# Kernel optimization log

Measured on AMD Instinct MI355X. Metric: run time of the kernel, lower is better.

Reference implementation:

```python
import jax, jax.numpy as jnp
import numpy as np

N_NODES = 100000
N_EDGES = 1600000
IN_F = 256
OUT_F = 128


def setup_inputs() -> dict:
    key = jax.random.key(0)
    k1, k2, k3, k4, k5, k6 = jax.random.split(key, 6)
    X_input = jax.random.normal(k1, (N_NODES, IN_F), dtype=jnp.float32)
    adj_row = jax.random.randint(k2, (N_EDGES,), 0, N_NODES, dtype=jnp.int32)
    adj_col = jax.random.randint(k3, (N_EDGES,), 0, N_NODES, dtype=jnp.int32)
    adj_val = jax.random.uniform(k4, (N_EDGES,), dtype=jnp.float32)
    W = jax.random.normal(k5, (IN_F, OUT_F), dtype=jnp.float32) / np.sqrt(IN_F)
    bias = jax.random.normal(k6, (OUT_F,), dtype=jnp.float32) * 0.01
    return {"X_input": X_input, "adj_row": adj_row, "adj_col": adj_col,
            "adj_val": adj_val, "W": W, "bias": bias}


def reference(X_input, adj_row, adj_col, adj_val, W, bias):
    # dense linear (no bias): support = X @ W   [N, out]
    support = X_input @ W
    # sparse adjacency matmul (COO spmm): out[r] += val * support[c]
    messages = adj_val[:, None] * support[adj_col]          # [E, out]
    output = jax.ops.segment_sum(messages, adj_row, num_segments=N_NODES)
    return output + bias
```

## Files before the change

kernel.cpp:

```cpp
#include <hip/hip_runtime.h>

#define N_NODES 100000
#define N_EDGES 1600000
#define IN_F    256
#define OUT_F   128

#define BROWS    128
#define NB       782
#define CAP      2560
#define PART_EPB 8192

typedef __attribute__((ext_vector_type(8))) short   s16x8;
typedef __attribute__((ext_vector_type(4))) float   f32x4;
typedef __attribute__((ext_vector_type(8))) unsigned short u16x8;

__device__ __forceinline__ unsigned short f2bf(float f) {
    unsigned u = __float_as_uint(f);
    u += 0x7FFFu + ((u >> 16) & 1u);
    return (unsigned short)(u >> 16);
}
__device__ __forceinline__ float bf2f(unsigned short h) {
    return __uint_as_float((unsigned)h << 16);
}

__global__ __launch_bounds__(256) void wt_build(const float* __restrict__ W,
                                                unsigned short* __restrict__ Wt) {
    const int n = blockIdx.x;
    const int k = threadIdx.x;
    Wt[n * IN_F + k] = f2bf(W[(size_t)k * OUT_F + n]);
}

__global__ __launch_bounds__(256) void gemm_mfma(const float* __restrict__ X,
                                                 const unsigned short* __restrict__ Wt,
                                                 unsigned short* __restrict__ support) {
    __shared__ unsigned short As[64][40];
    __shared__ unsigned short Bs[128][40];
    __shared__ unsigned short Ct[64][136];

    const int t    = threadIdx.x;
    const int wid  = t >> 6;
    const int lane = t & 63;
    const int tm   = lane & 15;
    const int quad = lane >> 4;
    const int row0 = blockIdx.x * 64;

    f32x4 acc[8];
#pragma unroll
    for (int c = 0; c < 8; ++c) acc[c] = (f32x4){0.f, 0.f, 0.f, 0.f};

    for (int kb = 0; kb < IN_F; kb += 32) {
        {
            const int m  = t >> 2;
            const int k0 = (t & 3) * 8;
            const int gr = row0 + m;
            float4 x0 = make_float4(0.f, 0.f, 0.f, 0.f), x1 = x0;
            if (gr < N_NODES) {
                const float* xp = &X[(size_t)gr * IN_F + kb + k0];
                x0 = *(const float4*)xp;
                x1 = *(const float4*)(xp + 4);
            }
            ushort4 a0, a1;
            a0.x = f2bf(x0.x); a0.y = f2bf(x0.y); a0.z = f2bf(x0.z); a0.w = f2bf(x0.w);
            a1.x = f2bf(x1.x); a1.y = f2bf(x1.y); a1.z = f2bf(x1.z); a1.w = f2bf(x1.w);
            *(ushort4*)&As[m][k0]     = a0;
            *(ushort4*)&As[m][k0 + 4] = a1;
        }
        {
            const int n  = t >> 1;
            const int k0 = (t & 1) * 16;
            const unsigned short* wp = &Wt[(size_t)n * IN_F + kb + k0];
            *(u16x8*)&Bs[n][k0]     = *(const u16x8*)wp;
            *(u16x8*)&Bs[n][k0 + 8] = *(const u16x8*)(wp + 8);
        }
        __syncthreads();

        const s16x8 a = *(const s16x8*)&As[wid * 16 + tm][quad * 8];
#pragma unroll
        for (int c = 0; c < 8; ++c) {
            const s16x8 b = *(const s16x8*)&Bs[c * 16 + tm][quad * 8];
            acc[c] = __builtin_amdgcn_mfma_f32_16x16x32_bf16(a, b, acc[c], 0, 0, 0);
        }
        __syncthreads();
    }

#pragma unroll
    for (int c = 0; c < 8; ++c) {
        const int col = c * 16 + tm;
#pragma unroll
        for (int reg = 0; reg < 4; ++reg) {
            const int m = wid * 16 + quad * 4 + reg;
            Ct[m][col] = f2bf(acc[c][reg]);
        }
    }
    __syncthreads();
    {
        const int m   = t >> 2;
        const int seg = (t & 3) * 32;
        const int gr  = row0 + m;
        if (gr < N_NODES) {
            unsigned short* op = &support[(size_t)gr * OUT_F + seg];
#pragma unroll
            for (int i = 0; i < 4; ++i)
                *(u16x8*)(op + i * 8) = *(const u16x8*)&Ct[m][seg + i * 8];
        }
    }
}

__global__ __launch_bounds__(256) void zero_cursor(int* __restrict__ cursor) {
    const int i = blockIdx.x * 256 + threadIdx.x;
    if (i < NB) cursor[i] = 0;
}

__global__ __launch_bounds__(256) void partition_edges(const int* __restrict__ arow,
                                                       const int* __restrict__ acol,
                                                       const float* __restrict__ aval,
                                                       int* __restrict__ cursor,
                                                       int2* __restrict__ epackA) {
    __shared__ int cnt[NB];
    __shared__ int basep[NB];
    const int t = threadIdx.x;
    for (int k = t; k < NB; k += 256) cnt[k] = 0;
    __syncthreads();
    const int base = blockIdx.x * PART_EPB;
    const int lim  = min(base + PART_EPB, N_EDGES);
    for (int i = base + t; i < lim; i += 256) atomicAdd(&cnt[arow[i] >> 7], 1);
    __syncthreads();
    for (int k = t; k < NB; k += 256) {
        const int c = cnt[k];
        if (c > 0) basep[k] = atomicAdd(&cursor[k], c);
        cnt[k] = 0;
    }
    __syncthreads();
    for (int i = base + t; i < lim; i += 256) {
        const int r    = arow[i];
        const int b    = r >> 7;
        const int rank = atomicAdd(&cnt[b], 1);
        const int pos  = basep[b] + rank;
        if (pos < CAP)
            epackA[(size_t)b * CAP + pos] =
                make_int2(((r & (BROWS - 1)) << 17) | acol[i], __float_as_int(aval[i]));
    }
}

__global__ __launch_bounds__(256) void bucket_csr(const int* __restrict__ cursor,
                                                  const int2* __restrict__ epackA,
                                                  int2* __restrict__ rowmeta,
                                                  int2* __restrict__ epackB) {
    __shared__ int rcnt[BROWS];
    __shared__ int incl[BROWS];
    __shared__ int rcur[BROWS];
    const int b = blockIdx.x;
    const int t = threadIdx.x;
    const int s = b * CAP;
    const int n = min(cursor[b], CAP);

    if (t < BROWS) rcnt[t] = 0;
    __syncthreads();
    for (int i = t; i < n; i += 256) atomicAdd(&rcnt[epackA[s + i].x >> 17], 1);
    __syncthreads();

    if (t < BROWS) {
        const int lane = t & 63;
        int x = rcnt[t];
#pragma unroll
        for (int off = 1; off < 64; off <<= 1) {
            const int y = __shfl_up(x, off, 64);
            if (lane >= off) x += y;
        }
        incl[t] = x;
    }
    __syncthreads();
    if (t < BROWS) {
        const int excl = incl[t] - rcnt[t] + (t >= 64 ? incl[63] : 0);
        rcur[t] = excl;
        const int r = (b << 7) + t;
        if (r < N_NODES) rowmeta[r] = make_int2(s + excl, rcnt[t]);
    }
    __syncthreads();

    for (int i = t; i < n; i += 256) {
        const int2 ep  = epackA[s + i];
        const int  rl  = ep.x >> 17;
        const int  pos = atomicAdd(&rcur[rl], 1);
        epackB[s + pos] = make_int2(ep.x & 0x1FFFF, ep.y);
    }
}

__global__ __launch_bounds__(256) void csr_gather(const int2* __restrict__ rowmeta,
                                                  const int2* __restrict__ epackB,
                                                  const unsigned short* __restrict__ support,
                                                  const float* __restrict__ bias,
                                                  float* __restrict__ out) {
    const int t = threadIdx.x;
    const int g = t >> 5;
    const int l = t & 31;
    const int r = blockIdx.x * 8 + g;
    if (r >= N_NODES) return;

    const int2 rm   = rowmeta[r];
    const int start = rm.x;
    const int deg   = rm.y;

    float4 acc = *(const float4*)&bias[l * 4];

    int i = 0;
    for (; i + 4 <= deg; i += 4) {
        const int2 e0 = epackB[start + i + 0];
        const int2 e1 = epackB[start + i + 1];
        const int2 e2 = epackB[start + i + 2];
        const int2 e3 = epackB[start + i + 3];
        const ushort4 u0 = *(const ushort4*)&support[(size_t)e0.x * OUT_F + l * 4];
        const ushort4 u1 = *(const ushort4*)&support[(size_t)e1.x * OUT_F + l * 4];
        const ushort4 u2 = *(const ushort4*)&support[(size_t)e2.x * OUT_F + l * 4];
        const ushort4 u3 = *(const ushort4*)&support[(size_t)e3.x * OUT_F + l * 4];
        const float v0 = __int_as_float(e0.y);
        const float v1 = __int_as_float(e1.y);
        const float v2 = __int_as_float(e2.y);
        const float v3 = __int_as_float(e3.y);
        acc.x = fmaf(v0, bf2f(u0.x), fmaf(v1, bf2f(u1.x), fmaf(v2, bf2f(u2.x), fmaf(v3, bf2f(u3.x), acc.x))));
        acc.y = fmaf(v0, bf2f(u0.y), fmaf(v1, bf2f(u1.y), fmaf(v2, bf2f(u2.y), fmaf(v3, bf2f(u3.y), acc.y))));
        acc.z = fmaf(v0, bf2f(u0.z), fmaf(v1, bf2f(u1.z), fmaf(v2, bf2f(u2.z), fmaf(v3, bf2f(u3.z), acc.z))));
        acc.w = fmaf(v0, bf2f(u0.w), fmaf(v1, bf2f(u1.w), fmaf(v2, bf2f(u2.w), fmaf(v3, bf2f(u3.w), acc.w))));
    }
    for (; i < deg; ++i) {
        const int2 e = epackB[start + i];
        const ushort4 u = *(const ushort4*)&support[(size_t)e.x * OUT_F + l * 4];
        const float v = __int_as_float(e.y);
        acc.x = fmaf(v, bf2f(u.x), acc.x);
        acc.y = fmaf(v, bf2f(u.y), acc.y);
        acc.z = fmaf(v, bf2f(u.z), acc.z);
        acc.w = fmaf(v, bf2f(u.w), acc.w);
    }

    *(float4*)&out[(size_t)r * OUT_F + l * 4] = acc;
}

extern "C" void kernel_launch(void* const* d_in, const int* in_sizes, int n_in,
                              void* d_out, int out_size, void* d_ws, size_t ws_size,
                              hipStream_t stream) {
    const float* X    = (const float*)d_in[0];
    const int*   arow = (const int*)d_in[1];
    const int*   acol = (const int*)d_in[2];
    const float* aval = (const float*)d_in[3];
    const float* W    = (const float*)d_in[4];
    const float* bias = (const float*)d_in[5];
    float*       out  = (float*)d_out;

    char* ws = (char*)d_ws;
    unsigned short* support = (unsigned short*)ws;  ws += (size_t)N_NODES * OUT_F * 2;
    int2*  rowmeta = (int2*)ws;                     ws += (size_t)N_NODES * 8;
    unsigned short* Wt = (unsigned short*)ws;       ws += (size_t)IN_F * OUT_F * 2;
    int*   cursor  = (int*)ws;                      ws += ((NB + 7) & ~7) * 4;
    int2*  epackB  = (int2*)ws;
    int2*  epackA  = (int2*)d_out;

    wt_build<<<OUT_F, 256, 0, stream>>>(W, Wt);
    zero_cursor<<<4, 256, 0, stream>>>(cursor);
    gemm_mfma<<<(N_NODES + 63) / 64, 256, 0, stream>>>(X, Wt, support);
    partition_edges<<<(N_EDGES + PART_EPB - 1) / PART_EPB, 256, 0, stream>>>(
        arow, acol, aval, cursor, epackA);
    bucket_csr<<<NB, 256, 0, stream>>>(cursor, epackA, rowmeta, epackB);
    csr_gather<<<(N_NODES + 7) / 8, 256, 0, stream>>>(
        rowmeta, epackB, support, bias, out);
}
```

Before: 320.8 us.

## Build CSR via global row histogram, three-pass scan, and atomic scatter

Replaces the two-level bucket partition (bucket buckets of 128 rows with fixed capacity, then per-bucket sort) with a direct COO-to-CSR conversion. A global per-row histogram is built with atomics, then a three-kernel prefix scan produces row offsets, and edges are scattered to their final positions with global atomic cursors. This removes the intermediate epackA pass and the capacity cap, and it fuses zeroing of the row counters into wt_build. In exchange it adds more kernel launches and more global atomic traffic spread over 100k counters.

```diff
diff --git a/kernel.cpp b/kernel.cpp
--- a/kernel.cpp
+++ b/kernel.cpp
@@ -5,10 +5,9 @@
 #define IN_F    256
 #define OUT_F   128
 
-#define BROWS    128
-#define NB       782
-#define CAP      2560
-#define PART_EPB 8192
+#define NPAD      100352
+#define SCAN_NBLK 98
+#define HIST_EPB  4096
 
 typedef __attribute__((ext_vector_type(8))) short   s16x8;
 typedef __attribute__((ext_vector_type(4))) float   f32x4;
@@ -24,10 +23,13 @@
 }
 
 __global__ __launch_bounds__(256) void wt_build(const float* __restrict__ W,
-                                                unsigned short* __restrict__ Wt) {
+                                                unsigned short* __restrict__ Wt,
+                                                int* __restrict__ rowcnt) {
     const int n = blockIdx.x;
     const int k = threadIdx.x;
     Wt[n * IN_F + k] = f2bf(W[(size_t)k * OUT_F + n]);
+    for (int i = blockIdx.x * 256 + threadIdx.x; i < NPAD; i += OUT_F * 256)
+        rowcnt[i] = 0;
 }
 
 __global__ __launch_bounds__(256) void gemm_mfma(const float* __restrict__ X,
@@ -106,83 +108,95 @@
     }
 }
 
-__global__ __launch_bounds__(256) void zero_cursor(int* __restrict__ cursor) {
-    const int i = blockIdx.x * 256 + threadIdx.x;
-    if (i < NB) cursor[i] = 0;
-}
-
-__global__ __launch_bounds__(256) void partition_edges(const int* __restrict__ arow,
-                                                       const int* __restrict__ acol,
-                                                       const float* __restrict__ aval,
-                                                       int* __restrict__ cursor,
-                                                       int2* __restrict__ epackA) {
-    __shared__ int cnt[NB];
-    __shared__ int basep[NB];
-    const int t = threadIdx.x;
-    for (int k = t; k < NB; k += 256) cnt[k] = 0;
+__global__ __launch_bounds__(256) void hist(const int* __restrict__ arow,
+                                            int* __restrict__ rowcnt) {
+    const int base = blockIdx.x * HIST_EPB;
+    const int lim  = min(base + HIST_EPB, N_EDGES);
+    for (int i = base + threadIdx.x; i < lim; i += 256)
+        atomicAdd(&rowcnt[arow[i]], 1);
+}
+
+__global__ __launch_bounds__(256) void scan1(const int* __restrict__ rowcnt,
+                                             int* __restrict__ tmp,
+                                             int* __restrict__ btot) {
+    __shared__ int wsum[4];
+    const int t  = threadIdx.x;
+    const int i0 = blockIdx.x * 1024 + t * 4;
+    const int4 v = *(const int4*)&rowcnt[i0];
+    const int tsum = v.x + v.y + v.z + v.w;
+    const int lane = t & 63;
+    int x = tsum;
+#pragma unroll
+    for (int off = 1; off < 64; off <<= 1) {
+        const int y = __shfl_up(x, off, 64);
+        if (lane >= off) x += y;
+    }
+    if (lane == 63) wsum[t >> 6] = x;
     __syncthreads();
-    const int base = blockIdx.x * PART_EPB;
-    const int lim  = min(base + PART_EPB, N_EDGES);
-    for (int i = base + t; i < lim; i += 256) atomicAdd(&cnt[arow[i] >> 7], 1);
+    int pre = x - tsum;
+    const int w = t >> 6;
+    for (int k = 0; k < w; ++k) pre += wsum[k];
+    int4 o;
+    o.x = pre;
+    o.y = pre + v.x;
+    o.z = o.y + v.y;
+    o.w = o.z + v.z;
+    *(int4*)&tmp[i0] = o;
+    if (t == 255) btot[blockIdx.x] = pre + tsum;
+}
+
+__global__ __launch_bounds__(128) void scan2(const int* __restrict__ btot,
+                                             int* __restrict__ boffs) {
+    __shared__ int s[128];
+    const int t  = threadIdx.x;
+    const int my = (t < SCAN_NBLK) ? btot[t] : 0;
+    s[t] = my;
     __syncthreads();
-    for (int k = t; k < NB; k += 256) {
-        const int c = cnt[k];
-        if (c > 0) basep[k] = atomicAdd(&cursor[k], c);
-        cnt[k] = 0;
-    }
-    __syncthreads();
-    for (int i = base + t; i < lim; i += 256) {
-        const int r    = arow[i];
-        const int b    = r >> 7;
-        const int rank = atomicAdd(&cnt[b], 1);
-        const int pos  = basep[b] + rank;
-        if (pos < CAP)
-            epackA[(size_t)b * CAP + pos] =
-                make_int2(((r & (BROWS - 1)) << 17) | acol[i], __float_as_int(aval[i]));
-    }
-}
-
-__global__ __launch_bounds__(256) void bucket_csr(const int* __restrict__ cursor,
-                                                  const int2* __restrict__ epackA,
-                                                  int2* __restrict__ rowmeta,
-                                                  int2* __restrict__ epackB) {
-    __shared__ int rcnt[BROWS];
-    __shared__ int incl[BROWS];
-    __shared__ int rcur[BROWS];
-    const int b = blockIdx.x;
-    const int t = threadIdx.x;
-    const int s = b * CAP;
-    const int n = min(cursor[b], CAP);
-
-    if (t < BROWS) rcnt[t] = 0;
-    __syncthreads();
-    for (int i = t; i < n; i += 256) atomicAdd(&rcnt[epackA[s + i].x >> 17], 1);
-    __syncthreads();
-
-    if (t < BROWS) {
-        const int lane = t & 63;
-        int x = rcnt[t];
-#pragma unroll
-        for (int off = 1; off < 64; off <<= 1) {
-            const int y = __shfl_up(x, off, 64);
-            if (lane >= off) x += y;
-        }
-        incl[t] = x;
-    }
-    __syncthreads();
-    if (t < BROWS) {
-        const int excl = incl[t] - rcnt[t] + (t >= 64 ? incl[63] : 0);
-        rcur[t] = excl;
-        const int r = (b << 7) + t;
-        if (r < N_NODES) rowmeta[r] = make_int2(s + excl, rcnt[t]);
-    }
-    __syncthreads();
-
-    for (int i = t; i < n; i += 256) {
-        const int2 ep  = epackA[s + i];
-        const int  rl  = ep.x >> 17;
-        const int  pos = atomicAdd(&rcur[rl], 1);
-        epackB[s + pos] = make_int2(ep.x & 0x1FFFF, ep.y);
+    for (int off = 1; off < 128; off <<= 1) {
+        const int add = (t >= off) ? s[t - off] : 0;
+        __syncthreads();
+        s[t] += add;
+        __syncthreads();
+    }
+    if (t < SCAN_NBLK) boffs[t] = s[t] - my;
+}
+
+__global__ __launch_bounds__(256) void scan3(const int* __restrict__ rowcnt,
+                                             const int* __restrict__ tmp,
+                                             const int* __restrict__ boffs,
+                                             int2* __restrict__ rowmeta,
+                                             int* __restrict__ cursor) {
+    const int t  = threadIdx.x;
+    const int i0 = blockIdx.x * 1024 + t * 4;
+    const int bo = boffs[blockIdx.x];
+    const int4 v = *(const int4*)&rowcnt[i0];
+    const int4 p = *(const int4*)&tmp[i0];
+    const int4 st = make_int4(p.x + bo, p.y + bo, p.z + bo, p.w + bo);
+    *(int4*)&cursor[i0] = st;
+    if (i0 + 3 < N_NODES) {
+        const int4 m0 = make_int4(st.x, v.x, st.y, v.y);
+        const int4 m1 = make_int4(st.z, v.z, st.w, v.w);
+        *(int4*)&rowmeta[i0]     = m0;
+        *(int4*)&rowmeta[i0 + 2] = m1;
+    } else {
+        const int sa[4] = {st.x, st.y, st.z, st.w};
+        const int va[4] = {v.x, v.y, v.z, v.w};
+        for (int j = 0; j < 4; ++j)
+            if (i0 + j < N_NODES) rowmeta[i0 + j] = make_int2(sa[j], va[j]);
+    }
+}
+
+__global__ __launch_bounds__(256) void scatter_edges(const int* __restrict__ arow,
+                                                     const int* __restrict__ acol,
+                                                     const float* __restrict__ aval,
+                                                     int* __restrict__ cursor,
+                                                     int2* __restrict__ epackB) {
+    const int base = blockIdx.x * HIST_EPB;
+    const int lim  = min(base + HIST_EPB, N_EDGES);
+    for (int i = base + threadIdx.x; i < lim; i += 256) {
+        const int r   = arow[i];
+        const int pos = atomicAdd(&cursor[r], 1);
+        epackB[pos] = make_int2(acol[i], __float_as_int(aval[i]));
     }
 }
 
@@ -248,18 +262,23 @@
 
     char* ws = (char*)d_ws;
     unsigned short* support = (unsigned short*)ws;  ws += (size_t)N_NODES * OUT_F * 2;
-    int2*  rowmeta = (int2*)ws;                     ws += (size_t)N_NODES * 8;
     unsigned short* Wt = (unsigned short*)ws;       ws += (size_t)IN_F * OUT_F * 2;
-    int*   cursor  = (int*)ws;                      ws += ((NB + 7) & ~7) * 4;
-    int2*  epackB  = (int2*)ws;
-    int2*  epackA  = (int2*)d_out;
-
-    wt_build<<<OUT_F, 256, 0, stream>>>(W, Wt);
-    zero_cursor<<<4, 256, 0, stream>>>(cursor);
+    int*  rowcnt  = (int*)ws;                       ws += (size_t)NPAD * 4;
+    int*  tmp     = (int*)ws;                       ws += (size_t)NPAD * 4;
+    int*  cursor  = (int*)ws;                       ws += (size_t)NPAD * 4;
+    int*  btot    = (int*)ws;                       ws += 128 * 4;
+    int*  boffs   = (int*)ws;                       ws += 128 * 4;
+    int2* rowmeta = (int2*)ws;                      ws += (size_t)N_NODES * 8;
+    int2* epackB  = (int2*)ws;
+
+    wt_build<<<OUT_F, 256, 0, stream>>>(W, Wt, rowcnt);
     gemm_mfma<<<(N_NODES + 63) / 64, 256, 0, stream>>>(X, Wt, support);
-    partition_edges<<<(N_EDGES + PART_EPB - 1) / PART_EPB, 256, 0, stream>>>(
-        arow, acol, aval, cursor, epackA);
-    bucket_csr<<<NB, 256, 0, stream>>>(cursor, epackA, rowmeta, epackB);
+    hist<<<(N_EDGES + HIST_EPB - 1) / HIST_EPB, 256, 0, stream>>>(arow, rowcnt);
+    scan1<<<SCAN_NBLK, 256, 0, stream>>>(rowcnt, tmp, btot);
+    scan2<<<1, 128, 0, stream>>>(btot, boffs);
+    scan3<<<SCAN_NBLK, 256, 0, stream>>>(rowcnt, tmp, boffs, rowmeta, cursor);
+    scatter_edges<<<(N_EDGES + HIST_EPB - 1) / HIST_EPB, 256, 0, stream>>>(
+        arow, acol, aval, cursor, epackB);
     csr_gather<<<(N_NODES + 7) / 8, 256, 0, stream>>>(
         rowmeta, epackB, support, bias, out);
 }
```

New measurement: 437.2 us. 36.3% more time.

## Register-cache edges in partition and bucket passes, widen buckets to 256 rows

Applied to the files above, without the earlier changes.

Partition and bucket kernels now load each edge once into registers and reuse the shared-memory atomic rank, instead of re-reading the input and redoing atomics in a second pass. Buckets widen to 256 rows (391 buckets, cap 4800) and partition blocks shrink to 4096 edges. The cursor zeroing is folded into wt_build to drop a launch. This cuts global reads and atomic traffic in the CSR build, at the cost of more registers per thread. Larger buckets also risk overflowing the cap, which would silently drop edges.

```diff
diff --git a/kernel.cpp b/kernel.cpp
--- a/kernel.cpp
+++ b/kernel.cpp
@@ -5,10 +5,12 @@
 #define IN_F    256
 #define OUT_F   128
 
-#define BROWS    128
-#define NB       782
-#define CAP      2560
-#define PART_EPB 8192
+#define BROWS2   256
+#define NB2      391
+#define CAPB     4800
+#define PART_EPB 4096
+#define KE       (PART_EPB / 256)
+#define KB       ((CAPB + 255) / 256)
 
 typedef __attribute__((ext_vector_type(8))) short   s16x8;
 typedef __attribute__((ext_vector_type(4))) float   f32x4;
@@ -24,10 +26,13 @@
 }
 
 __global__ __launch_bounds__(256) void wt_build(const float* __restrict__ W,
-                                                unsigned short* __restrict__ Wt) {
+                                                unsigned short* __restrict__ Wt,
+                                                int* __restrict__ cursorA) {
     const int n = blockIdx.x;
     const int k = threadIdx.x;
     Wt[n * IN_F + k] = f2bf(W[(size_t)k * OUT_F + n]);
+    const int idx = blockIdx.x * 256 + threadIdx.x;
+    if (idx < NB2) cursorA[idx] = 0;
 }
 
 __global__ __launch_bounds__(256) void gemm_mfma(const float* __restrict__ X,
@@ -106,83 +111,103 @@
     }
 }
 
-__global__ __launch_bounds__(256) void zero_cursor(int* __restrict__ cursor) {
-    const int i = blockIdx.x * 256 + threadIdx.x;
-    if (i < NB) cursor[i] = 0;
-}
-
 __global__ __launch_bounds__(256) void partition_edges(const int* __restrict__ arow,
                                                        const int* __restrict__ acol,
                                                        const float* __restrict__ aval,
-                                                       int* __restrict__ cursor,
+                                                       int* __restrict__ cursorA,
                                                        int2* __restrict__ epackA) {
-    __shared__ int cnt[NB];
-    __shared__ int basep[NB];
+    __shared__ int cnt[NB2];
+    __shared__ int basep[NB2];
     const int t = threadIdx.x;
-    for (int k = t; k < NB; k += 256) cnt[k] = 0;
-    __syncthreads();
+    for (int k = t; k < NB2; k += 256) cnt[k] = 0;
+    __syncthreads();
+
     const int base = blockIdx.x * PART_EPB;
-    const int lim  = min(base + PART_EPB, N_EDGES);
-    for (int i = base + t; i < lim; i += 256) atomicAdd(&cnt[arow[i] >> 7], 1);
-    __syncthreads();
-    for (int k = t; k < NB; k += 256) {
+    int pk_[KE], vv_[KE], b_[KE], rk_[KE];
+#pragma unroll
+    for (int k = 0; k < KE; ++k) {
+        const int i = base + t + k * 256;
+        b_[k] = -1;
+        if (i < N_EDGES) {
+            const int r = arow[i];
+            b_[k]  = r >> 8;
+            pk_[k] = ((r & (BROWS2 - 1)) << 17) | acol[i];
+            vv_[k] = __float_as_int(aval[i]);
+            rk_[k] = atomicAdd(&cnt[b_[k]], 1);
+        }
+    }
+    __syncthreads();
+    for (int k = t; k < NB2; k += 256) {
         const int c = cnt[k];
-        if (c > 0) basep[k] = atomicAdd(&cursor[k], c);
-        cnt[k] = 0;
-    }
-    __syncthreads();
-    for (int i = base + t; i < lim; i += 256) {
-        const int r    = arow[i];
-        const int b    = r >> 7;
-        const int rank = atomicAdd(&cnt[b], 1);
-        const int pos  = basep[b] + rank;
-        if (pos < CAP)
-            epackA[(size_t)b * CAP + pos] =
-                make_int2(((r & (BROWS - 1)) << 17) | acol[i], __float_as_int(aval[i]));
-    }
-}
-
-__global__ __launch_bounds__(256) void bucket_csr(const int* __restrict__ cursor,
-                                                  const int2* __restrict__ epackA,
-                                                  int2* __restrict__ rowmeta,
-                                                  int2* __restrict__ epackB) {
-    __shared__ int rcnt[BROWS];
-    __shared__ int incl[BROWS];
-    __shared__ int rcur[BROWS];
+        if (c > 0) basep[k] = atomicAdd(&cursorA[k], c);
+    }
+    __syncthreads();
+#pragma unroll
+    for (int k = 0; k < KE; ++k) {
+        if (b_[k] >= 0) {
+            const int pos = basep[b_[k]] + rk_[k];
+            if (pos < CAPB)
+                epackA[(size_t)b_[k] * CAPB + pos] = make_int2(pk_[k], vv_[k]);
+        }
+    }
+}
+
+__global__ __launch_bounds__(256) void bucket_build(const int* __restrict__ cursorA,
+                                                    const int2* __restrict__ epackA,
+                                                    int2* __restrict__ rowmeta,
+                                                    int2* __restrict__ epackB) {
+    __shared__ int cnt[BROWS2];
+    __shared__ int excl[BROWS2];
+    __shared__ int wsum[4];
     const int b = blockIdx.x;
     const int t = threadIdx.x;
-    const int s = b * CAP;
-    const int n = min(cursor[b], CAP);
-
-    if (t < BROWS) rcnt[t] = 0;
-    __syncthreads();
-    for (int i = t; i < n; i += 256) atomicAdd(&rcnt[epackA[s + i].x >> 17], 1);
-    __syncthreads();
-
-    if (t < BROWS) {
+    cnt[t] = 0;
+    __syncthreads();
+
+    const size_t sa = (size_t)b * CAPB;
+    const int n = min(cursorA[b], CAPB);
+
+    int pk_[KB], vv_[KB], rk_[KB];
+#pragma unroll
+    for (int k = 0; k < KB; ++k) {
+        const int i = t + k * 256;
+        rk_[k] = -1;
+        if (i < n) {
+            const int2 e = epackA[sa + i];
+            pk_[k] = e.x;
+            vv_[k] = e.y;
+            rk_[k] = atomicAdd(&cnt[e.x >> 17], 1);
+        }
+    }
+    __syncthreads();
+
+    {
         const int lane = t & 63;
-        int x = rcnt[t];
+        const int my   = cnt[t];
+        int x = my;
 #pragma unroll
         for (int off = 1; off < 64; off <<= 1) {
             const int y = __shfl_up(x, off, 64);
             if (lane >= off) x += y;
         }
-        incl[t] = x;
-    }
-    __syncthreads();
-    if (t < BROWS) {
-        const int excl = incl[t] - rcnt[t] + (t >= 64 ? incl[63] : 0);
-        rcur[t] = excl;
-        const int r = (b << 7) + t;
-        if (r < N_NODES) rowmeta[r] = make_int2(s + excl, rcnt[t]);
-    }
-    __syncthreads();
-
-    for (int i = t; i < n; i += 256) {
-        const int2 ep  = epackA[s + i];
-        const int  rl  = ep.x >> 17;
-        const int  pos = atomicAdd(&rcur[rl], 1);
-        epackB[s + pos] = make_int2(ep.x & 0x1FFFF, ep.y);
+        if (lane == 63) wsum[t >> 6] = x;
+        __syncthreads();
+        int pre = x - my;
+        const int w = t >> 6;
+        for (int kk = 0; kk < w; ++kk) pre += wsum[kk];
+        excl[t] = pre;
+        const int r = b * BROWS2 + t;
+        if (r < N_NODES) rowmeta[r] = make_int2((int)sa + pre, my);
+    }
+    __syncthreads();
+
+#pragma unroll
+    for (int k = 0; k < KB; ++k) {
+        if (rk_[k] >= 0) {
+            const int rl  = pk_[k] >> 17;
+            const int pos = excl[rl] + rk_[k];
+            epackB[sa + pos] = make_int2(pk_[k] & 0x1FFFF, vv_[k]);
+        }
     }
 }
 
@@ -248,18 +273,17 @@
 
     char* ws = (char*)d_ws;
     unsigned short* support = (unsigned short*)ws;  ws += (size_t)N_NODES * OUT_F * 2;
-    int2*  rowmeta = (int2*)ws;                     ws += (size_t)N_NODES * 8;
     unsigned short* Wt = (unsigned short*)ws;       ws += (size_t)IN_F * OUT_F * 2;
-    int*   cursor  = (int*)ws;                      ws += ((NB + 7) & ~7) * 4;
-    int2*  epackB  = (int2*)ws;
-    int2*  epackA  = (int2*)d_out;
-
-    wt_build<<<OUT_F, 256, 0, stream>>>(W, Wt);
-    zero_cursor<<<4, 256, 0, stream>>>(cursor);
+    int2* rowmeta = (int2*)ws;                      ws += (size_t)N_NODES * 8;
+    int*  cursorA = (int*)ws;                       ws += ((NB2 + 7) & ~7) * 4;
+    int2* epackB  = (int2*)ws;
+    int2* epackA  = (int2*)d_out;
+
+    wt_build<<<OUT_F, 256, 0, stream>>>(W, Wt, cursorA);
     gemm_mfma<<<(N_NODES + 63) / 64, 256, 0, stream>>>(X, Wt, support);
     partition_edges<<<(N_EDGES + PART_EPB - 1) / PART_EPB, 256, 0, stream>>>(
-        arow, acol, aval, cursor, epackA);
-    bucket_csr<<<NB, 256, 0, stream>>>(cursor, epackA, rowmeta, epackB);
+        arow, acol, aval, cursorA, epackA);
+    bucket_build<<<NB2, 256, 0, stream>>>(cursorA, epackA, rowmeta, epackB);
     csr_gather<<<(N_NODES + 7) / 8, 256, 0, stream>>>(
         rowmeta, epackB, support, bias, out);
 }
```

After: 289.4 us. 9.8% less time.
